# Performance work log

Hardware: AMD Instinct MI355X
Metric: run time of the kernel (lower is better)

## Reference

```python
import jax, jax.numpy as jnp
import numpy as np

B, T = 8, 2048
DV, DA = 1024, 128          # visual / audio feature dims
D1, D2 = 512, 128           # conv1d channels
DH = D2 + DA + 1            # 257: lorentz dim after time-coord pad
DG = 128                    # per-branch GCN output dim (args.dim)
NEG = 0.01                  # LeakyReLU slope
K_CURV = 1.0
EPS = 1e-6


def leaky(x):
    return jnp.where(x >= 0, x, NEG * x)


def expmap0_lorentz(x):
    # x: [B,T,DH] with x[...,0] == 0 (tangent at origin), k = 1
    xs = x[..., 1:]
    n = jnp.sqrt(jnp.maximum(jnp.sum(xs * xs, -1, keepdims=True), 1e-12))
    return jnp.concatenate([jnp.cosh(n), jnp.sinh(n) / n * xs], axis=-1)


def lorentz_similarity(x):
    # xy_inner = -<x,x>_L  (negate time component of left factor, negate product)
    signs = jnp.concatenate([-jnp.ones((1,), x.dtype), jnp.ones((DH - 1,), x.dtype)])
    xy = -jnp.einsum('bid,bjd->bij', x * signs, x)          # [B,T,T]
    xy = jnp.maximum(xy, 1.0)                                # F.threshold(., 1, 1)
    d = (K_CURV ** 0.5) * jnp.log(xy + jnp.sqrt(xy * xy - 1.0 + 1e-7))
    return jnp.clip(d, EPS, 200.0)


def adj_fn(proj_x, seq_len):
    x2 = jnp.exp(-lorentz_similarity(proj_x))               # [B,T,T]
    pos = jnp.arange(T)
    row = pos[None, :, None] < seq_len[:, None, None]       # [B,T,1]
    col = pos[None, None, :] < seq_len[:, None, None]       # [B,1,T]
    thr = jnp.where(x2 > 0.8, x2, 0.0)                      # F.threshold(., 0.8, 0)
    logits = jnp.where(col, thr, -1e30)                     # softmax over valid cols
    p = jax.nn.softmax(logits, axis=-1)
    return p * (row & col)                                  # zero outside [:L,:L]


def clas_fn(logits, seq_len):
    # logits: [B,T]; per-sample top-k (k = L//16 + 1) mean, then sigmoid
    pos = jnp.arange(T)
    valid = pos[None, :] < seq_len[:, None]
    masked = jnp.where(valid, logits, -1e30)
    srt = -jnp.sort(-masked, axis=1)                         # descending
    k = seq_len // 16 + 1                                    # [B]
    kmask = pos[None, :] < k[:, None]
    mil = jnp.sum(srt * kmask, axis=1) / k.astype(logits.dtype)
    return jax.nn.sigmoid(mil)


def forward(inputs, seq_len, w1, b1, w2, b2, gw1, gw2, cls_w, cls_b):
    xv = inputs[:, :, :DV]
    xa = inputs[:, :, DV:]
    xv = leaky(jnp.einsum('btc,oc->bto', xv, w1) + b1)       # conv1d k=1
    xv = leaky(jnp.einsum('btc,oc->bto', xv, w2) + b2)
    x = jnp.concatenate([xv, xa], axis=-1)                   # [B,T,256]

    # DistanceAdj: exp(-|i-j| / e), shared across batch
    pos = jnp.arange(T, dtype=jnp.float32)
    disadj = jnp.exp(-jnp.abs(pos[:, None] - pos[None, :]) / jnp.exp(1.0))  # [T,T]

    # expm: pad time coord, lorentz expmap0
    proj_x = expmap0_lorentz(
        jnp.concatenate([jnp.zeros(x.shape[:-1] + (1,), x.dtype), x], axis=-1))  # [B,T,257]

    adj = adj_fn(proj_x, seq_len)                            # [B,T,T]

    x1 = leaky(jnp.einsum('bij,bjd->bid', adj, proj_x) @ gw1)        # HFSGCN stand-in
    x2 = leaky(jnp.einsum('ij,bjd->bid', disadj, proj_x) @ gw2)      # HTRGCN stand-in
    out_x = jnp.concatenate([x1, x2], axis=-1)               # [B,T,256]

    # HypClassifier: 2 + 2*<x, cls>_L + bias  (lorentz inner)
    signs = jnp.concatenate([-jnp.ones((1,), out_x.dtype), jnp.ones((2 * DG - 1,), out_x.dtype)])
    frame_prob = 2.0 + 2.0 * jnp.einsum('btd,cd->btc', out_x * signs, cls_w) + cls_b  # [B,T,1]

    mil_logits = clas_fn(frame_prob[..., 0], seq_len)        # [B]
    return mil_logits, frame_prob


def setup_inputs() -> dict:
    key = jax.random.key(0)
    ks = jax.random.split(key, 8)
    inputs = jax.random.normal(ks[0], (B, T, DV + DA), jnp.float32)
    seq_len = jax.random.randint(ks[1], (B,), T // 2, T + 1, jnp.int32)
    w1 = jax.random.normal(ks[2], (D1, DV), jnp.float32) / np.float32(np.sqrt(DV))
    b1 = jnp.zeros((D1,), jnp.float32)
    w2 = jax.random.normal(ks[3], (D2, D1), jnp.float32) / np.float32(np.sqrt(D1))
    b2 = jnp.zeros((D2,), jnp.float32)
    gw1 = jax.random.normal(ks[4], (DH, DG), jnp.float32) / np.float32(np.sqrt(DH))
    gw2 = jax.random.normal(ks[5], (DH, DG), jnp.float32) / np.float32(np.sqrt(DH))
    cls_w = jax.random.normal(ks[6], (1, 2 * DG), jnp.float32) / np.float32(np.sqrt(2 * DG))
    cls_b = jnp.zeros((1,), jnp.float32)
    return dict(inputs=inputs, seq_len=seq_len, w1=w1, b1=b1, w2=w2, b2=b2,
                gw1=gw1, gw2=gw2, cls_w=cls_w, cls_b=cls_b)


def reference(inputs, seq_len, w1, b1, w2, b2, gw1, gw2, cls_w, cls_b):
    return forward(inputs, seq_len, w1, b1, w2, b2, gw1, gw2, cls_w, cls_b)
```

## Files before the change

### kernel.cpp

```cpp
#include <hip/hip_runtime.h>
#include <math.h>

#define BB 8
#define TT 2048
#define DV_ 1024
#define DA_ 128
#define D1_ 512
#define D2_ 128
#define DH_ 257
#define DHP 288
#define DG_ 128
#define MTOT (BB*TT)
#define NPX ((size_t)MTOT*DHP)

#define NEGS 0.01f
#define INV_E 0.36787944117144233f
#define CH 64
#define HALO 64
#define UB 8

#define RS 40
#define BKC 32

static const size_t o_big = 0;
static const size_t o_c1  = 16777216;
static const size_t o_c2  = o_c1 + 8388608;
static const size_t o_w   = o_c2 + 2097152;
static const size_t o_S   = o_w + 663552;
static const size_t o_den = o_S + 2304;

static const size_t sw_w1h = 0;
static const size_t sw_w1l = 524288;
static const size_t sw_w2h = 1048576;
static const size_t sw_w2l = 1114112;
static const size_t sw_g1h = 1179648;
static const size_t sw_g1l = 1216512;
static const size_t sw_g2h = 1253376;
static const size_t sw_g2l = 1290240;

typedef __attribute__((ext_vector_type(8))) __bf16 bf16x8;
typedef __attribute__((ext_vector_type(8))) unsigned short us8;
typedef __attribute__((ext_vector_type(4))) float f32x4;

__device__ __forceinline__ float diag_w() {
    float dd = logf(1.0f + sqrtf(1.0f*1.0f - 1.0f + 1e-7f));
    dd = fminf(fmaxf(dd, 1e-6f), 200.0f);
    float x2 = expf(-dd);
    return expf(x2) - 1.0f;
}

__device__ __forceinline__ unsigned short f2bf(float f) {
    unsigned int u = __float_as_uint(f);
    u += 0x7FFFu + ((u >> 16) & 1u);
    return (unsigned short)(u >> 16);
}
__device__ __forceinline__ float bf2f(unsigned short h) {
    return __uint_as_float((unsigned int)h << 16);
}

__device__ __forceinline__ void cvt8(const float4 a, const float4 b,
                                     us8& h, us8& l) {
    unsigned short hh;
#define CV_(idx, val) hh = f2bf(val); h[idx] = hh; l[idx] = f2bf((val) - bf2f(hh));
    CV_(0, a.x) CV_(1, a.y) CV_(2, a.z) CV_(3, a.w)
    CV_(4, b.x) CV_(5, b.y) CV_(6, b.z) CV_(7, b.w)
#undef CV_
}

__global__ void k_setup(float* __restrict__ den, const int* __restrict__ seq,
                        float* __restrict__ S,
                        const float* __restrict__ w1, const float* __restrict__ w2,
                        unsigned short* __restrict__ h1, unsigned short* __restrict__ l1,
                        unsigned short* __restrict__ h2, unsigned short* __restrict__ l2,
                        const float* __restrict__ g1, const float* __restrict__ g2,
                        unsigned short* __restrict__ gh1, unsigned short* __restrict__ gl1,
                        unsigned short* __restrict__ gh2, unsigned short* __restrict__ gl2)
{
    const int bx = blockIdx.x;
    if (bx < 64) {
        int r = bx * 256 + threadIdx.x;
        den[r] = (float)seq[r >> 11] + diag_w();
        if (r < BB * DHP) S[r] = 0.f;
    } else if (bx < 640) {
        size_t i = ((size_t)(bx - 64) * 256 + threadIdx.x) * 4;
        const float* src; unsigned short *h, *l; size_t o;
        if (i < (size_t)D1_ * DV_) { src = w1; h = h1; l = l1; o = i; }
        else {
            o = i - (size_t)D1_ * DV_;
            if (o >= (size_t)D2_ * D1_) return;
            src = w2; h = h2; l = l2;
        }
        float4 v = *(const float4*)(src + o);
        ushort4 hv, lv;
        hv.x = f2bf(v.x); lv.x = f2bf(v.x - bf2f(hv.x));
        hv.y = f2bf(v.y); lv.y = f2bf(v.y - bf2f(hv.y));
        hv.z = f2bf(v.z); lv.z = f2bf(v.z - bf2f(hv.z));
        hv.w = f2bf(v.w); lv.w = f2bf(v.w - bf2f(hv.w));
        *(ushort4*)(h + o) = hv;
        *(ushort4*)(l + o) = lv;
    } else {
        const int bb = bx - 640;
        const int zz = (bb >= 144);
        int i = (bb - (zz ? 144 : 0)) * 256 + threadIdx.x;
        if (i >= DG_ * DHP) return;
        const float* g = zz ? g2 : g1;
        unsigned short* th = zz ? gh2 : gh1;
        unsigned short* tl = zz ? gl2 : gl1;
        int c = i / DHP, k = i - c * DHP;
        float v = (k < DH_) ? g[k * DG_ + c] : 0.f;
        unsigned short hh = f2bf(v);
        th[i] = hh;
        tl[i] = f2bf(v - bf2f(hh));
    }
}

__global__ __launch_bounds__(512, 2) void gemm_mlp1(
    const float* __restrict__ inA,
    const unsigned short* __restrict__ Bh, const unsigned short* __restrict__ Bl,
    const float* __restrict__ bias,
    unsigned short* __restrict__ Ch, unsigned short* __restrict__ Cl)
{
    __shared__ unsigned short sm[2][2][128 * RS];
    const int ib = blockIdx.x;
    const int x = ib & 7, slot = ib >> 3;
    const int cc = slot & 3, g = slot >> 2;
    const int row0 = (x + 8 * g) * 128, col0 = cc * 128;
    const int tid = threadIdx.x;
    const int wave = tid >> 6, lane = tid & 63;
    const int r0w = (wave >> 2) * 64;
    const int c0 = col0 + (wave & 3) * 32;
    const int q = lane >> 4, m = lane & 15;
    const int srow = tid >> 2, scol = (tid & 3) << 3;
    const size_t gA0 = (size_t)(row0 + srow) * 1152 + scol;
    const int s0 = srow * RS + scol;
    size_t bo_[2];
#pragma unroll
    for (int t = 0; t < 2; ++t) bo_[t] = (size_t)(c0 + t*16 + m) * DV_ + q*8;

    float4 a00, a01;
    bf16x8 fah[4], fal[4];
    bf16x8 bh0[2], bl0[2], bh1[2], bl1[2];

#define M1_LDGA(o) { \
    a00 = *(const float4*)(inA + gA0 + (o)); a01 = *(const float4*)(inA + gA0 + (o) + 4); }
#define M1_STAGE(BUF) { \
    us8 h_, l_; \
    cvt8(a00, a01, h_, l_); \
    *(us8*)&sm[BUF][0][s0] = h_; *(us8*)&sm[BUF][1][s0] = l_; }
#define M1_LDGB(S, o) \
    _Pragma("unroll") \
    for (int t = 0; t < 2; ++t) { \
        bh##S[t] = *(const bf16x8*)(Bh + bo_[t] + (o)); \
        bl##S[t] = *(const bf16x8*)(Bl + bo_[t] + (o)); }
#define M1_LOADA(BUF) \
    _Pragma("unroll") \
    for (int t = 0; t < 4; ++t) { \
        const int ra = (r0w + t*16 + m) * RS + q*8; \
        fah[t] = *(const bf16x8*)&sm[BUF][0][ra]; \
        fal[t] = *(const bf16x8*)&sm[BUF][1][ra]; }
#define M1_MFMA(S) \
    _Pragma("unroll") \
    for (int mi = 0; mi < 4; ++mi) \
        _Pragma("unroll") \
        for (int nj = 0; nj < 2; ++nj) { \
            acc[mi][nj] = __builtin_amdgcn_mfma_f32_16x16x32_bf16(fah[mi], bh##S[nj], acc[mi][nj], 0, 0, 0); \
            acc[mi][nj] = __builtin_amdgcn_mfma_f32_16x16x32_bf16(fal[mi], bh##S[nj], acc[mi][nj], 0, 0, 0); \
            acc[mi][nj] = __builtin_amdgcn_mfma_f32_16x16x32_bf16(fah[mi], bl##S[nj], acc[mi][nj], 0, 0, 0); \
        }

    f32x4 acc[4][2];
#pragma unroll
    for (int a = 0; a < 4; ++a)
#pragma unroll
        for (int c = 0; c < 2; ++c) acc[a][c] = (f32x4){0.f, 0.f, 0.f, 0.f};

    M1_LDGA(0)
    M1_STAGE(0)
    M1_LDGB(0, 0)
    __syncthreads();

    const int NI = (DV_ / BKC) / 2;
    for (int i = 0; i < NI; ++i) {
        const size_t o1 = (size_t)(2*i + 1) * BKC;
        M1_LDGA(o1)
        M1_LDGB(1, o1)
        M1_LOADA(0)
        M1_MFMA(0)
        M1_STAGE(1)
        __syncthreads();
        if (i + 1 < NI) {
            const size_t o2 = (size_t)(2*i + 2) * BKC;
            M1_LDGA(o2)
            M1_LDGB(0, o2)
        }
        M1_LOADA(1)
        M1_MFMA(1)
        if (i + 1 < NI) { M1_STAGE(0) }
        __syncthreads();
    }
#undef M1_LDGA
#undef M1_STAGE
#undef M1_LDGB
#undef M1_LOADA
#undef M1_MFMA

    float bj[2];
#pragma unroll
    for (int nj = 0; nj < 2; ++nj) bj[nj] = bias[c0 + nj*16 + m];
#pragma unroll
    for (int mi = 0; mi < 4; ++mi)
#pragma unroll
        for (int nj = 0; nj < 2; ++nj)
#pragma unroll
            for (int t = 0; t < 4; ++t) {
                int i = row0 + r0w + mi*16 + q*4 + t;
                int j = c0 + nj*16 + m;
                float v = acc[mi][nj][t] + bj[nj];
                v = (v >= 0.f) ? v : NEGS * v;
                size_t o = (size_t)i * D1_ + j;
                unsigned short hh = f2bf(v);
                Ch[o] = hh;
                Cl[o] = f2bf(v - bf2f(hh));
            }
}

#define LOADK(S, k0) \
    _Pragma("unroll") \
    for (int t = 0; t < 4; ++t) { \
        size_t ao = (size_t)(r0 + t*16 + m) * lda + (k0) + q*8; \
        size_t bo = (size_t)(c0 + t*16 + m) * ldb + (k0) + q*8; \
        ah##S[t] = *(const bf16x8*)(Ah + ao); \
        al##S[t] = *(const bf16x8*)(Al + ao); \
        bh##S[t] = *(const bf16x8*)(Bh + bo); \
        bl##S[t] = *(const bf16x8*)(Bl + bo); \
    }
#define MFMAK(S) \
    _Pragma("unroll") \
    for (int mi = 0; mi < 4; ++mi) \
        _Pragma("unroll") \
        for (int nj = 0; nj < 4; ++nj) { \
            acc[mi][nj] = __builtin_amdgcn_mfma_f32_16x16x32_bf16(ah##S[mi], bh##S[nj], acc[mi][nj], 0, 0, 0); \
            acc[mi][nj] = __builtin_amdgcn_mfma_f32_16x16x32_bf16(al##S[mi], bh##S[nj], acc[mi][nj], 0, 0, 0); \
            acc[mi][nj] = __builtin_amdgcn_mfma_f32_16x16x32_bf16(ah##S[mi], bl##S[nj], acc[mi][nj], 0, 0, 0); \
        }

#define LOADK2(S, k0, LD) \
    _Pragma("unroll") \
    for (int t = 0; t < 4; ++t) { \
        size_t ao = (size_t)(r0 + t*16 + m) * (LD) + (k0) + q*8; \
        ah##S[t] = *(const bf16x8*)(Ah + ao); \
        al##S[t] = *(const bf16x8*)(Al + ao); \
    } \
    _Pragma("unroll") \
    for (int t = 0; t < 2; ++t) { \
        size_t bo = (size_t)(c0 + t*16 + m) * (LD) + (k0) + q*8; \
        bh##S[t] = *(const bf16x8*)(Bh + bo); \
        bl##S[t] = *(const bf16x8*)(Bl + bo); \
    }
#define MFMAK2(S) \
    _Pragma("unroll") \
    for (int mi = 0; mi < 4; ++mi) \
        _Pragma("unroll") \
        for (int nj = 0; nj < 2; ++nj) { \
            acc[mi][nj] = __builtin_amdgcn_mfma_f32_16x16x32_bf16(ah##S[mi], bh##S[nj], acc[mi][nj], 0, 0, 0); \
            acc[mi][nj] = __builtin_amdgcn_mfma_f32_16x16x32_bf16(al##S[mi], bh##S[nj], acc[mi][nj], 0, 0, 0); \
            acc[mi][nj] = __builtin_amdgcn_mfma_f32_16x16x32_bf16(ah##S[mi], bl##S[nj], acc[mi][nj], 0, 0, 0); \
        }

__global__ __launch_bounds__(256, 1) void gemm_mlp2(
    const unsigned short* __restrict__ Ah, const unsigned short* __restrict__ Al,
    const unsigned short* __restrict__ Bh, const unsigned short* __restrict__ Bl,
    const float* __restrict__ bias, float* __restrict__ Cf)
{
    const int row0 = blockIdx.x * 64;
    const int wave = threadIdx.x >> 6, lane = threadIdx.x & 63;
    const int r0 = row0, c0 = wave * 32;
    const int q = lane >> 4, m = lane & 15;
    f32x4 acc[4][2];
#pragma unroll
    for (int a = 0; a < 4; ++a)
#pragma unroll
        for (int c = 0; c < 2; ++c) acc[a][c] = (f32x4){0.f, 0.f, 0.f, 0.f};
    bf16x8 ah0[4], al0[4], bh0[2], bl0[2];
    bf16x8 ah1[4], al1[4], bh1[2], bl1[2];
    LOADK2(0, 0, D1_)
    for (int k0 = 0; k0 + 64 <= D1_; k0 += 64) {
        LOADK2(1, k0 + 32, D1_)
        MFMAK2(0)
        if (k0 + 64 < D1_) { LOADK2(0, k0 + 64, D1_) }
        MFMAK2(1)
    }
    float bj[2];
#pragma unroll
    for (int nj = 0; nj < 2; ++nj) bj[nj] = bias[c0 + nj*16 + m];
#pragma unroll
    for (int mi = 0; mi < 4; ++mi)
#pragma unroll
        for (int nj = 0; nj < 2; ++nj)
#pragma unroll
            for (int t = 0; t < 4; ++t) {
                int i = r0 + mi*16 + q*4 + t;
                int j = c0 + nj*16 + m;
                float v = acc[mi][nj][t] + bj[nj];
                v = (v >= 0.f) ? v : NEGS * v;
                Cf[(size_t)i * D2_ + j] = v;
            }
}

__global__ __launch_bounds__(256, 1) void gemm_gc(
    const unsigned short* __restrict__ A1h, const unsigned short* __restrict__ A1l,
    const unsigned short* __restrict__ A2h, const unsigned short* __restrict__ A2l,
    const unsigned short* __restrict__ G1h, const unsigned short* __restrict__ G1l,
    const unsigned short* __restrict__ G2h, const unsigned short* __restrict__ G2l,
    float* __restrict__ X1, float* __restrict__ X2)
{
    const int z = blockIdx.z;
    const unsigned short* Ah = z ? A2h : A1h;
    const unsigned short* Al = z ? A2l : A1l;
    const unsigned short* Bh = z ? G2h : G1h;
    const unsigned short* Bl = z ? G2l : G1l;
    float* Cf = z ? X2 : X1;
    const int lda = DHP, ldb = DHP;
    const int row0 = blockIdx.y * 128, col0 = 0;
    const int wave = threadIdx.x >> 6, lane = threadIdx.x & 63;
    const int r0 = row0 + (wave >> 1) * 64, c0 = col0 + (wave & 1) * 64;
    const int q = lane >> 4, m = lane & 15;
    f32x4 acc[4][4];
#pragma unroll
    for (int a = 0; a < 4; ++a)
#pragma unroll
        for (int c = 0; c < 4; ++c) acc[a][c] = (f32x4){0.f, 0.f, 0.f, 0.f};
    bf16x8 ah0[4], al0[4], bh0[4], bl0[4];
    bf16x8 ah1[4], al1[4], bh1[4], bl1[4];
    LOADK(0, 0)
    int k0 = 0;
    for (; k0 + 64 <= DHP; k0 += 64) {
        LOADK(1, k0 + 32)
        MFMAK(0)
        if (k0 + 64 < DHP) { LOADK(0, k0 + 64) }
        MFMAK(1)
    }
    if (k0 < DHP) { MFMAK(0) }
#pragma unroll
    for (int mi = 0; mi < 4; ++mi)
#pragma unroll
        for (int nj = 0; nj < 4; ++nj)
#pragma unroll
            for (int t = 0; t < 4; ++t) {
                int i = r0 + mi*16 + q*4 + t;
                int j = c0 + nj*16 + m;
                float v = acc[mi][nj][t];
                v = (v >= 0.f) ? v : NEGS * v;
                Cf[(size_t)i * DG_ + j] = v;
            }
}

#define XLOAD(S, k0) \
    _Pragma("unroll") \
    for (int t = 0; t < 4; ++t) { \
        af##S[t] = *(const bf16x8*)(base + (size_t)(r0 + t*16 + m) * DHP + (k0) + q*8); \
        bf##S[t] = *(const bf16x8*)(base + (size_t)(c0 + t*16 + m) * DHP + (k0) + q*8); \
    }
#define XMFMA(S) \
    _Pragma("unroll") \
    for (int mi = 0; mi < 4; ++mi) \
        _Pragma("unroll") \
        for (int nj = 0; nj < 4; ++nj) \
            acc[mi][nj] = __builtin_amdgcn_mfma_f32_16x16x32_bf16(af##S[mi], bf##S[nj], acc[mi][nj], 0, 0, 0);

__global__ __launch_bounds__(256, 1) void k_xy_mfma(
    const unsigned short* __restrict__ pxb, const float* __restrict__ px,
    const int* __restrict__ seq, float* __restrict__ den, float* __restrict__ accb)
{
    const int b = blockIdx.z;
    const int bx = blockIdx.x, by = blockIdx.y;
    if (bx < by) return;
    const int nb = seq[b];
    const int row0 = by * 128, col0 = bx * 128;
    if (row0 >= nb || col0 >= nb) return;
    const int wave = threadIdx.x >> 6, lane = threadIdx.x & 63;
    const int r0 = row0 + (wave >> 1) * 64, c0 = col0 + (wave & 1) * 64;
    if (c0 + 63 < r0 || r0 >= nb || c0 >= nb) return;
    const unsigned short* base = pxb + (size_t)b * TT * DHP;
    const int q = lane >> 4, m = lane & 15;
    f32x4 acc[4][4];
#pragma unroll
    for (int a = 0; a < 4; ++a)
#pragma unroll
        for (int c = 0; c < 4; ++c) acc[a][c] = (f32x4){0.f, 0.f, 0.f, 0.f};
    bf16x8 af0[4], bf0[4], af1[4], bf1[4];
    XLOAD(0, 0)
    int k0 = 0;
    for (; k0 + 64 <= DHP; k0 += 64) {
        XLOAD(1, k0 + 32)
        XMFMA(0)
        if (k0 + 64 < DHP) { XLOAD(0, k0 + 64) }
        XMFMA(1)
    }
    if (k0 < DHP) { XMFMA(0) }
    const float* b32 = px + (size_t)b * TT * DHP;
    float cj[4], ci[4][4];
#pragma unroll
    for (int nj = 0; nj < 4; ++nj) cj[nj] = b32[(size_t)(c0 + nj*16 + m) * DHP];
#pragma unroll
    for (int mi = 0; mi < 4; ++mi)
#pragma unroll
        for (int t = 0; t < 4; ++t) ci[mi][t] = b32[(size_t)(r0 + mi*16 + q*4 + t) * DHP];
#pragma unroll
    for (int mi = 0; mi < 4; ++mi)
#pragma unroll
        for (int nj = 0; nj < 4; ++nj)
#pragma unroll
            for (int t = 0; t < 4; ++t) {
                int i = r0 + mi*16 + q*4 + t;
                int j = c0 + nj*16 + m;
                if (i < j && j < nb) {
                    float xyv = 2.f * ci[mi][t] * cj[nj] - acc[mi][nj][t];
                    float xym = fmaxf(xyv, 1.0f);
                    if (xym < 1.026f) {
                        float dd = logf(xym + sqrtf(xym * xym - 1.0f + 1e-7f));
                        dd = fminf(fmaxf(dd, 1e-6f), 200.0f);
                        float x2v = expf(-dd);
                        if (x2v > 0.8f) {
                            float w = expf(x2v) - 1.0f;
                            atomicAdd(&den[b * TT + i], w);
                            atomicAdd(&den[b * TT + j], w);
                            const float* pi = b32 + (size_t)i * DHP;
                            const float* pj = b32 + (size_t)j * DHP;
                            float* ai = accb + ((size_t)(b * TT + i)) * DHP;
                            float* aj = accb + ((size_t)(b * TT + j)) * DHP;
                            for (int d = 0; d < DHP; ++d) {
                                atomicAdd(&ai[d], w * pj[d]);
                                atomicAdd(&aj[d], w * pi[d]);
                            }
                        }
                    }
                }
            }
}

__global__ __launch_bounds__(256) void k_proj(
    const float* __restrict__ C2, const float* __restrict__ inputs,
    float* __restrict__ px, unsigned short* __restrict__ pxb,
    float* __restrict__ accb)
{
    const int r = blockIdx.x;
    const int tid = threadIdx.x;
    float v = (tid < 128) ? C2[(size_t)r * 128 + tid]
                          : inputs[(size_t)r * 1152 + 1024 + (tid - 128)];
    float sq = v * v;
#pragma unroll
    for (int o = 32; o > 0; o >>= 1) sq += __shfl_down(sq, o, 64);
    __shared__ float wred[4];
    __shared__ float cs[2];
    if ((tid & 63) == 0) wred[tid >> 6] = sq;
    __syncthreads();
    if (tid == 0) {
        float n2 = fmaxf(wred[0] + wred[1] + wred[2] + wred[3], 1e-12f);
        float n = sqrtf(n2);
        cs[0] = coshf(n);
        cs[1] = sinhf(n) / n;
    }
    __syncthreads();
    float sv = cs[1] * v;
    px[(size_t)r * DHP + 1 + tid] = sv;
    pxb[(size_t)r * DHP + 1 + tid] = f2bf(sv);
    if (tid == 0) {
        px[(size_t)r * DHP] = cs[0];
        pxb[(size_t)r * DHP] = f2bf(cs[0]);
    }
    if (tid < DHP - DH_) {
        px[(size_t)r * DHP + DH_ + tid] = 0.f;
        pxb[(size_t)r * DHP + DH_ + tid] = 0;
    }
    float* ab = accb + (size_t)r * DHP;
    ab[tid] = 0.f;
    if (tid < DHP - 256) ab[256 + tid] = 0.f;
}

__global__ __launch_bounds__(256) void k_ssum(
    const float* __restrict__ px, const int* __restrict__ seq,
    float* __restrict__ S)
{
    const int b = blockIdx.x, chunk = blockIdx.y, tid = threadIdx.x;
    const int nb = seq[b];
    const int j0 = chunk * 32;
    const int j1 = (j0 + 32 < nb) ? j0 + 32 : nb;
    float a0 = 0.f, a1 = 0.f;
    const bool hasB = (tid < DHP - 256);
    for (int j = j0; j < j1; ++j) {
        const float* row = px + ((size_t)(b * TT + j)) * DHP;
        a0 += row[tid];
        if (hasB) a1 += row[256 + tid];
    }
    if (j1 > j0) {
        atomicAdd(&S[b * DHP + tid], a0);
        if (hasB) atomicAdd(&S[b * DHP + 256 + tid], a1);
    }
}

__global__ void k_y1(const float* __restrict__ accb, const float* __restrict__ S,
                     const float* __restrict__ den, const int* __restrict__ seq,
                     const float* __restrict__ px,
                     unsigned short* __restrict__ yh, unsigned short* __restrict__ yl)
{
    size_t idx = (size_t)blockIdx.x * 256 + threadIdx.x;
    if (idx >= NPX) return;
    int r = (int)(idx / DHP);
    int b = r >> 11, i = r & (TT - 1);
    int d = (int)(idx - (size_t)r * DHP);
    float out = 0.f;
    if (i < seq[b])
        out = (S[b * DHP + d] + accb[idx] + diag_w() * px[idx]) / den[r];
    unsigned short hh = f2bf(out);
    yh[idx] = hh;
    yl[idx] = f2bf(out - bf2f(hh));
}

__global__ __launch_bounds__(256) void k_band(
    const float* __restrict__ px,
    unsigned short* __restrict__ yh, unsigned short* __restrict__ yl)
{
    __shared__ float Fs[CH][DHP];
    const int b = blockIdx.y;
    const int i0 = blockIdx.x * CH;
    const int tid = threadIdx.x;
    const bool hasB = (tid < DHP - 256);
    const float r = expf(-INV_E);
    const float* base = px + (size_t)b * TT * DHP;

    {
        const int jlo = (i0 - HALO > 0) ? i0 - HALO : 0;
        float LA = 0.f, LB = 0.f;
        for (int j = jlo; j < i0 + CH; j += UB) {
            float va[UB], vb[UB];
#pragma unroll
            for (int u = 0; u < UB; ++u) {
                const float* row = base + (size_t)(j + u) * DHP;
                va[u] = row[tid];
                vb[u] = hasB ? row[256 + tid] : 0.f;
            }
#pragma unroll
            for (int u = 0; u < UB; ++u) {
                LA = fmaf(r, LA, va[u]);
                LB = fmaf(r, LB, vb[u]);
                const int jj = j + u;
                if (jj >= i0) {
                    Fs[jj - i0][tid] = LA;
                    if (hasB) Fs[jj - i0][256 + tid] = LB;
                }
            }
        }
    }
    __syncthreads();
    {
        const int jhi = (i0 + CH - 1 + HALO < TT - 1) ? i0 + CH - 1 + HALO : TT - 1;
        float RA = 0.f, RB = 0.f;
        int j = jhi;
        for (; j >= i0 + CH; j -= UB) {
            float va[UB], vb[UB];
#pragma unroll
            for (int u = 0; u < UB; ++u) {
                const float* row = base + (size_t)(j - u) * DHP;
                va[u] = row[tid];
                vb[u] = hasB ? row[256 + tid] : 0.f;
            }
#pragma unroll
            for (int u = 0; u < UB; ++u) {
                RA = fmaf(r, RA, va[u]);
                RB = fmaf(r, RB, vb[u]);
            }
        }
        for (; j >= i0; j -= UB) {
            float va[UB], vb[UB];
#pragma unroll
            for (int u = 0; u < UB; ++u) {
                const float* row = base + (size_t)(j - u) * DHP;
                va[u] = row[tid];
                vb[u] = hasB ? row[256 + tid] : 0.f;
            }
#pragma unroll
            for (int u = 0; u < UB; ++u) {
                const int jj = j - u;
                RA = fmaf(r, RA, va[u]);
                RB = fmaf(r, RB, vb[u]);
                size_t o = ((size_t)(b * TT + jj)) * DHP + tid;
                float ya = Fs[jj - i0][tid] + RA - va[u];
                unsigned short hh = f2bf(ya);
                yh[o] = hh; yl[o] = f2bf(ya - bf2f(hh));
                if (hasB) {
                    float yb = Fs[jj - i0][256 + tid] + RB - vb[u];
                    size_t ob = o + 256;
                    unsigned short h2 = f2bf(yb);
                    yh[ob] = h2; yl[ob] = f2bf(yb - bf2f(h2));
                }
            }
        }
    }
}

__global__ __launch_bounds__(256) void k_frame(
    const float* __restrict__ x1, const float* __restrict__ x2f,
    const float* __restrict__ cls_w, const float* __restrict__ cls_b,
    float* __restrict__ dout)
{
    const int r = blockIdx.x * 4 + (threadIdx.x >> 6);
    const int lane = threadIdx.x & 63;
    float s = 0.f;
#pragma unroll
    for (int t = 0; t < 2; ++t) {
        int g = lane + t * 64;
        float cw1 = cls_w[g];
        if (g == 0) cw1 = -cw1;
        s += x1[(size_t)r * DG_ + g] * cw1;
        s += x2f[(size_t)r * DG_ + g] * cls_w[DG_ + g];
    }
#pragma unroll
    for (int o = 32; o > 0; o >>= 1) s += __shfl_down(s, o, 64);
    if (lane == 0) dout[8 + r] = 2.0f + 2.0f * s + cls_b[0];
}

__global__ __launch_bounds__(1024) void k_clas(
    const int* __restrict__ seq, float* __restrict__ dout)
{
    __shared__ float s[TT];
    const int b = blockIdx.x, tid = threadIdx.x;
    const int nb = seq[b];
    for (int t = tid; t < TT; t += 1024)
        s[t] = (t < nb) ? dout[8 + b * TT + t] : -1e30f;
    __syncthreads();
    for (int k = 2; k <= TT; k <<= 1)
        for (int j = k >> 1; j > 0; j >>= 1) {
            for (int i = tid; i < TT; i += 1024) {
                int ixj = i ^ j;
                if (ixj > i) {
                    float a = s[i], c = s[ixj];
                    bool descBlk = ((i & k) == 0);
                    if (descBlk ? (a < c) : (a > c)) { s[i] = c; s[ixj] = a; }
                }
            }
            __syncthreads();
        }
    const int kk = nb / 16 + 1;
    float part = 0.f;
    for (int t = tid; t < kk; t += 1024) part += s[t];
#pragma unroll
    for (int o = 32; o > 0; o >>= 1) part += __shfl_down(part, o, 64);
    __shared__ float wred[16];
    if ((tid & 63) == 0) wred[tid >> 6] = part;
    __syncthreads();
    if (tid == 0) {
        float mil = 0.f;
#pragma unroll
        for (int t = 0; t < 16; ++t) mil += wred[t];
        mil /= (float)kk;
        dout[b] = 1.f / (1.f + expf(-mil));
    }
}

extern "C" void kernel_launch(void* const* d_in, const int* in_sizes, int n_in,
                              void* d_out, int out_size, void* d_ws, size_t ws_size,
                              hipStream_t stream) {
    (void)in_sizes; (void)n_in; (void)out_size; (void)ws_size;
    const float* inputs = (const float*)d_in[0];
    const int*   seq    = (const int*)d_in[1];
    const float* w1     = (const float*)d_in[2];
    const float* b1     = (const float*)d_in[3];
    const float* w2     = (const float*)d_in[4];
    const float* b2     = (const float*)d_in[5];
    const float* gw1    = (const float*)d_in[6];
    const float* gw2    = (const float*)d_in[7];
    const float* cls_w  = (const float*)d_in[8];
    const float* cls_b  = (const float*)d_in[9];
    float* dout = (float*)d_out;
    float* ws = (float*)d_ws;

    float* px  = ws + o_big;
    unsigned short* pxb = (unsigned short*)(ws + o_big + 4718592);
    unsigned short* y2h = (unsigned short*)(ws + o_big + 7077888);
    unsigned short* y2l = y2h + NPX;
    unsigned short* y1h = (unsigned short*)(ws + o_big + 11796480);
    unsigned short* y1l = y1h + NPX;
    unsigned short* C1h = (unsigned short*)(ws + o_c1);
    unsigned short* C1l = C1h + (size_t)MTOT * D1_;
    float* accb = ws + o_c1;
    float* x1   = ws + o_c1 + 4718592;
    float* C2  = ws + o_c2;
    float* x2f = ws + o_c2;
    unsigned short* wsS = (unsigned short*)(ws + o_w);
    unsigned short *W1h = wsS + sw_w1h, *W1l = wsS + sw_w1l;
    unsigned short *W2h = wsS + sw_w2h, *W2l = wsS + sw_w2l;
    unsigned short *g1h = wsS + sw_g1h, *g1l = wsS + sw_g1l;
    unsigned short *g2h = wsS + sw_g2h, *g2l = wsS + sw_g2l;
    float* S   = ws + o_S;
    float* den = ws + o_den;

    k_setup<<<928, 256, 0, stream>>>(den, seq, S, w1, w2, W1h, W1l, W2h, W2l,
                                     gw1, gw2, g1h, g1l, g2h, g2l);

    gemm_mlp1<<<512, 512, 0, stream>>>(inputs, W1h, W1l, b1, C1h, C1l);
    gemm_mlp2<<<256, 256, 0, stream>>>(C1h, C1l, W2h, W2l, b2, C2);

    k_proj<<<MTOT, 256, 0, stream>>>(C2, inputs, px, pxb, accb);

    k_ssum<<<dim3(BB, TT / 32), 256, 0, stream>>>(px, seq, S);

    k_xy_mfma<<<dim3(TT / 128, TT / 128, BB), 256, 0, stream>>>(pxb, px, seq, den, accb);

    k_y1<<<(int)(NPX / 256), 256, 0, stream>>>(accb, S, den, seq, px, y1h, y1l);

    k_band<<<dim3(TT / CH, BB), 256, 0, stream>>>(px, y2h, y2l);

    gemm_gc<<<dim3(1, MTOT / 128, 2), 256, 0, stream>>>(
        y1h, y1l, y2h, y2l, g1h, g1l, g2h, g2l, x1, x2f);

    k_frame<<<MTOT / 4, 256, 0, stream>>>(x1, x2f, cls_w, cls_b, dout);
    k_clas<<<BB, 1024, 0, stream>>>(seq, dout);
}
```

Before: 395.4 us.

## Rework proj to wave-per-row, split band by columns, radix-select top-k

k_proj now handles four rows per block with one wavefront per row, using a xor-shuffle reduction in place of shared memory and barriers. k_band splits the 288 feature columns into two 144-wide halves across a new grid z dimension, giving more blocks and no divergent second column group. It also drops the barrier between the forward and backward scans, which is safe because each thread only reads its own Fs column. k_clas replaces the full bitonic sort with an 8-bit radix-select threshold search and a sum of the elements above the threshold, with tie correction. The 192-thread band blocks leave 48 threads idle, and the radix select relies on shared-memory atomics.

```diff
diff --git a/kernel.cpp b/kernel.cpp
--- a/kernel.cpp
+++ b/kernel.cpp
@@ -444,38 +444,34 @@
     float* __restrict__ px, unsigned short* __restrict__ pxb,
     float* __restrict__ accb)
 {
-    const int r = blockIdx.x;
-    const int tid = threadIdx.x;
-    float v = (tid < 128) ? C2[(size_t)r * 128 + tid]
-                          : inputs[(size_t)r * 1152 + 1024 + (tid - 128)];
-    float sq = v * v;
-#pragma unroll
-    for (int o = 32; o > 0; o >>= 1) sq += __shfl_down(sq, o, 64);
-    __shared__ float wred[4];
-    __shared__ float cs[2];
-    if ((tid & 63) == 0) wred[tid >> 6] = sq;
-    __syncthreads();
-    if (tid == 0) {
-        float n2 = fmaxf(wred[0] + wred[1] + wred[2] + wred[3], 1e-12f);
-        float n = sqrtf(n2);
-        cs[0] = coshf(n);
-        cs[1] = sinhf(n) / n;
-    }
-    __syncthreads();
-    float sv = cs[1] * v;
-    px[(size_t)r * DHP + 1 + tid] = sv;
-    pxb[(size_t)r * DHP + 1 + tid] = f2bf(sv);
-    if (tid == 0) {
-        px[(size_t)r * DHP] = cs[0];
-        pxb[(size_t)r * DHP] = f2bf(cs[0]);
-    }
-    if (tid < DHP - DH_) {
-        px[(size_t)r * DHP + DH_ + tid] = 0.f;
-        pxb[(size_t)r * DHP + DH_ + tid] = 0;
-    }
-    float* ab = accb + (size_t)r * DHP;
-    ab[tid] = 0.f;
-    if (tid < DHP - 256) ab[256 + tid] = 0.f;
+    const int r = blockIdx.x * 4 + (threadIdx.x >> 6);
+    const int l = threadIdx.x & 63;
+    float v[4];
+#pragma unroll
+    for (int e = 0; e < 2; ++e)
+        v[e] = C2[(size_t)r * 128 + l + 64*e];
+#pragma unroll
+    for (int e = 2; e < 4; ++e)
+        v[e] = inputs[(size_t)r * 1152 + 1024 + (l + 64*e - 128)];
+    float sq = v[0]*v[0] + v[1]*v[1] + v[2]*v[2] + v[3]*v[3];
+#pragma unroll
+    for (int o = 32; o > 0; o >>= 1) sq += __shfl_xor(sq, o, 64);
+    float n2 = fmaxf(sq, 1e-12f);
+    float n = sqrtf(n2);
+    float cs0 = coshf(n);
+    float cs1 = sinhf(n) / n;
+    const size_t base = (size_t)r * DHP;
+#pragma unroll
+    for (int e = 0; e < 4; ++e) {
+        int idx = l + 64*e;
+        float sv = cs1 * v[e];
+        px[base + 1 + idx] = sv;
+        pxb[base + 1 + idx] = f2bf(sv);
+        accb[base + idx] = 0.f;
+    }
+    if (l == 0) { px[base] = cs0; pxb[base] = f2bf(cs0); }
+    if (l < DHP - DH_) { px[base + DH_ + l] = 0.f; pxb[base + DH_ + l] = 0; }
+    if (l < 32) accb[base + 256 + l] = 0.f;
 }
 
 __global__ __launch_bounds__(256) void k_ssum(
@@ -517,83 +513,60 @@
     yl[idx] = f2bf(out - bf2f(hh));
 }
 
-__global__ __launch_bounds__(256) void k_band(
+__global__ __launch_bounds__(192) void k_band(
     const float* __restrict__ px,
     unsigned short* __restrict__ yh, unsigned short* __restrict__ yl)
 {
-    __shared__ float Fs[CH][DHP];
+    __shared__ float Fs[CH][144];
     const int b = blockIdx.y;
     const int i0 = blockIdx.x * CH;
     const int tid = threadIdx.x;
-    const bool hasB = (tid < DHP - 256);
+    const int d = blockIdx.z * 144 + tid;
+    const bool act = (tid < 144);
     const float r = expf(-INV_E);
     const float* base = px + (size_t)b * TT * DHP;
 
-    {
+    if (act) {
         const int jlo = (i0 - HALO > 0) ? i0 - HALO : 0;
-        float LA = 0.f, LB = 0.f;
+        float LA = 0.f;
         for (int j = jlo; j < i0 + CH; j += UB) {
-            float va[UB], vb[UB];
-#pragma unroll
-            for (int u = 0; u < UB; ++u) {
-                const float* row = base + (size_t)(j + u) * DHP;
-                va[u] = row[tid];
-                vb[u] = hasB ? row[256 + tid] : 0.f;
-            }
+            float va[UB];
+#pragma unroll
+            for (int u = 0; u < UB; ++u)
+                va[u] = base[(size_t)(j + u) * DHP + d];
 #pragma unroll
             for (int u = 0; u < UB; ++u) {
                 LA = fmaf(r, LA, va[u]);
-                LB = fmaf(r, LB, vb[u]);
                 const int jj = j + u;
-                if (jj >= i0) {
-                    Fs[jj - i0][tid] = LA;
-                    if (hasB) Fs[jj - i0][256 + tid] = LB;
-                }
+                if (jj >= i0) Fs[jj - i0][tid] = LA;
             }
         }
     }
-    __syncthreads();
-    {
+    if (act) {
         const int jhi = (i0 + CH - 1 + HALO < TT - 1) ? i0 + CH - 1 + HALO : TT - 1;
-        float RA = 0.f, RB = 0.f;
+        float RA = 0.f;
         int j = jhi;
         for (; j >= i0 + CH; j -= UB) {
-            float va[UB], vb[UB];
-#pragma unroll
-            for (int u = 0; u < UB; ++u) {
-                const float* row = base + (size_t)(j - u) * DHP;
-                va[u] = row[tid];
-                vb[u] = hasB ? row[256 + tid] : 0.f;
-            }
-#pragma unroll
-            for (int u = 0; u < UB; ++u) {
-                RA = fmaf(r, RA, va[u]);
-                RB = fmaf(r, RB, vb[u]);
-            }
+            float va[UB];
+#pragma unroll
+            for (int u = 0; u < UB; ++u)
+                va[u] = base[(size_t)(j - u) * DHP + d];
+#pragma unroll
+            for (int u = 0; u < UB; ++u) RA = fmaf(r, RA, va[u]);
         }
         for (; j >= i0; j -= UB) {
-            float va[UB], vb[UB];
-#pragma unroll
-            for (int u = 0; u < UB; ++u) {
-                const float* row = base + (size_t)(j - u) * DHP;
-                va[u] = row[tid];
-                vb[u] = hasB ? row[256 + tid] : 0.f;
-            }
+            float va[UB];
+#pragma unroll
+            for (int u = 0; u < UB; ++u)
+                va[u] = base[(size_t)(j - u) * DHP + d];
 #pragma unroll
             for (int u = 0; u < UB; ++u) {
                 const int jj = j - u;
                 RA = fmaf(r, RA, va[u]);
-                RB = fmaf(r, RB, vb[u]);
-                size_t o = ((size_t)(b * TT + jj)) * DHP + tid;
+                size_t o = ((size_t)(b * TT + jj)) * DHP + d;
                 float ya = Fs[jj - i0][tid] + RA - va[u];
                 unsigned short hh = f2bf(ya);
                 yh[o] = hh; yl[o] = f2bf(ya - bf2f(hh));
-                if (hasB) {
-                    float yb = Fs[jj - i0][256 + tid] + RB - vb[u];
-                    size_t ob = o + 256;
-                    unsigned short h2 = f2bf(yb);
-                    yh[ob] = h2; yl[ob] = f2bf(yb - bf2f(h2));
-                }
             }
         }
     }
@@ -623,37 +596,75 @@
 __global__ __launch_bounds__(1024) void k_clas(
     const int* __restrict__ seq, float* __restrict__ dout)
 {
-    __shared__ float s[TT];
+    __shared__ unsigned su[TT];
+    __shared__ unsigned hist[256];
+    __shared__ unsigned sh_prefix;
+    __shared__ int sh_rem;
+    __shared__ float wred[16];
+    __shared__ int wcnt[16];
     const int b = blockIdx.x, tid = threadIdx.x;
     const int nb = seq[b];
-    for (int t = tid; t < TT; t += 1024)
-        s[t] = (t < nb) ? dout[8 + b * TT + t] : -1e30f;
+    const int kk = nb / 16 + 1;
+    for (int t = tid; t < TT; t += 1024) {
+        unsigned u = 0u;
+        if (t < nb) {
+            unsigned x = __float_as_uint(dout[8 + b * TT + t]);
+            u = (x & 0x80000000u) ? ~x : (x | 0x80000000u);
+        }
+        su[t] = u;
+    }
+    if (tid == 0) { sh_prefix = 0u; sh_rem = kk; }
     __syncthreads();
-    for (int k = 2; k <= TT; k <<= 1)
-        for (int j = k >> 1; j > 0; j >>= 1) {
-            for (int i = tid; i < TT; i += 1024) {
-                int ixj = i ^ j;
-                if (ixj > i) {
-                    float a = s[i], c = s[ixj];
-                    bool descBlk = ((i & k) == 0);
-                    if (descBlk ? (a < c) : (a > c)) { s[i] = c; s[ixj] = a; }
-                }
+#pragma unroll
+    for (int p = 0; p < 4; ++p) {
+        const int shift = 24 - 8 * p;
+        const unsigned hm = (p == 0) ? 0u : (0xFFFFFFFFu << (shift + 8));
+        if (tid < 256) hist[tid] = 0u;
+        __syncthreads();
+        const unsigned pref = sh_prefix;
+        for (int t = tid; t < TT; t += 1024) {
+            unsigned u = su[t];
+            if (u != 0u && (u & hm) == pref)
+                atomicAdd(&hist[(u >> shift) & 0xFFu], 1u);
+        }
+        __syncthreads();
+        if (tid == 0) {
+            int rem = sh_rem;
+            int v = 255;
+            for (; v > 0; --v) {
+                int c = (int)hist[v];
+                if (c < rem) rem -= c;
+                else break;
             }
-            __syncthreads();
-        }
-    const int kk = nb / 16 + 1;
-    float part = 0.f;
-    for (int t = tid; t < kk; t += 1024) part += s[t];
-#pragma unroll
-    for (int o = 32; o > 0; o >>= 1) part += __shfl_down(part, o, 64);
-    __shared__ float wred[16];
-    if ((tid & 63) == 0) wred[tid >> 6] = part;
+            sh_rem = rem;
+            sh_prefix = sh_prefix | ((unsigned)v << shift);
+        }
+        __syncthreads();
+    }
+    const unsigned T = sh_prefix;
+    float fsum = 0.f; int cnt = 0;
+    for (int t = tid; t < TT; t += 1024) {
+        unsigned u = su[t];
+        if (u > T) {
+            unsigned x = (u & 0x80000000u) ? (u ^ 0x80000000u) : ~u;
+            fsum += __uint_as_float(x);
+            ++cnt;
+        }
+    }
+#pragma unroll
+    for (int o = 32; o > 0; o >>= 1) {
+        fsum += __shfl_down(fsum, o, 64);
+        cnt  += __shfl_down(cnt, o, 64);
+    }
+    if ((tid & 63) == 0) { wred[tid >> 6] = fsum; wcnt[tid >> 6] = cnt; }
     __syncthreads();
     if (tid == 0) {
-        float mil = 0.f;
-#pragma unroll
-        for (int t = 0; t < 16; ++t) mil += wred[t];
-        mil /= (float)kk;
+        float s = 0.f; int c = 0;
+#pragma unroll
+        for (int t = 0; t < 16; ++t) { s += wred[t]; c += wcnt[t]; }
+        unsigned x = (T & 0x80000000u) ? (T ^ 0x80000000u) : ~T;
+        s += (float)(kk - c) * __uint_as_float(x);
+        float mil = s / (float)kk;
         dout[b] = 1.f / (1.f + expf(-mil));
     }
 }
@@ -701,7 +712,7 @@
     gemm_mlp1<<<512, 512, 0, stream>>>(inputs, W1h, W1l, b1, C1h, C1l);
     gemm_mlp2<<<256, 256, 0, stream>>>(C1h, C1l, W2h, W2l, b2, C2);
 
-    k_proj<<<MTOT, 256, 0, stream>>>(C2, inputs, px, pxb, accb);
+    k_proj<<<MTOT / 4, 256, 0, stream>>>(C2, inputs, px, pxb, accb);
 
     k_ssum<<<dim3(BB, TT / 32), 256, 0, stream>>>(px, seq, S);
 
@@ -709,7 +720,7 @@
 
     k_y1<<<(int)(NPX / 256), 256, 0, stream>>>(accb, S, den, seq, px, y1h, y1l);
 
-    k_band<<<dim3(TT / CH, BB), 256, 0, stream>>>(px, y2h, y2l);
+    k_band<<<dim3(TT / CH, BB, 2), 192, 0, stream>>>(px, y2h, y2l);
 
     gemm_gc<<<dim3(1, MTOT / 128, 2), 256, 0, stream>>>(
         y1h, y1l, y2h, y2l, g1h, g1l, g2h, g2l, x1, x2f);
```

After: 377.9 us. 1.05x faster.
